# Kernel tuning notes

Measured on AMD Instinct MI355X. Metric: run time of the kernel, lower is better.

The kernel has to match this reference:

```python
import jax, jax.numpy as jnp
import numpy as np

B = 16384
F_CONT = 128   # continuous features (Gaussian scopes)
F_CAT = 128    # integer-valued features (Categorical scopes)
NG = 1024      # number of Gaussian leaves
NC = 1024      # number of Categorical leaves
K = 32         # categorical classes
LOG_2PI = float(np.log(2.0 * np.pi))


def setup_inputs() -> dict:
    key = jax.random.key(0)
    k1, k2, k3, k4, k5, k6, k7 = jax.random.split(key, 7)
    # data: first F_CONT columns continuous, last F_CAT columns hold integer category values
    x_cont = jax.random.normal(k1, (B, F_CONT), dtype=jnp.float32)
    x_cat = jax.random.randint(k2, (B, F_CAT), 0, K).astype(jnp.float32)
    x = jnp.concatenate([x_cont, x_cat], axis=1)  # [B, 256]
    gauss_mean = jax.random.normal(k3, (NG,), dtype=jnp.float32)
    gauss_std = jax.random.uniform(k4, (NG,), dtype=jnp.float32, minval=0.5, maxval=2.0)
    cat_logp = jax.nn.log_softmax(jax.random.normal(k5, (NC, K), dtype=jnp.float32), axis=-1)
    gauss_scopes = jax.random.randint(k6, (NG,), 0, F_CONT)            # index into continuous cols
    cat_scopes = jax.random.randint(k7, (NC,), 0, F_CAT) + F_CONT      # index into categorical cols
    return {
        "x": x,
        "gauss_mean": gauss_mean,
        "gauss_std": gauss_std,
        "cat_logp": cat_logp,
        "gauss_scopes": gauss_scopes,
        "cat_scopes": cat_scopes,
    }


def reference(x, gauss_mean, gauss_std, cat_logp, gauss_scopes, cat_scopes):
    # Fused equivalent of the per-leaf Python loop: one gather + one formula per family.
    # Gaussian leaves: Normal(mean, std).log_prob(x[:, scope])
    gv = x[:, gauss_scopes]                                   # [B, NG]
    z = (gv - gauss_mean[None, :]) / gauss_std[None, :]
    g_ll = -0.5 * (z * z) - jnp.log(gauss_std)[None, :] - 0.5 * LOG_2PI
    # Categorical leaves: log p_i[x[:, scope_i]]
    cidx = x[:, cat_scopes].astype(jnp.int32)                 # [B, NC]
    c_ll = cat_logp[jnp.arange(cat_logp.shape[0])[None, :], cidx]  # [B, NC]
    return jnp.concatenate([g_ll, c_ll], axis=1)              # [B, NG+NC]
```

## Files before the change

### kernel.cpp

```cpp
#include <hip/hip_runtime.h>
#include <math.h>


#define HALF_LOG_2PI 0.91893853320467274178f

constexpr int BROWS   = 16384;
constexpr int FX      = 256;
constexpr int NG      = 1024;
constexpr int NC      = 1024;
constexpr int KCAT    = 32;
constexpr int OUTW    = NG + NC;
constexpr int ROWS_PB = 16;
constexpr int NTHR    = 256;
constexpr int XPITCH  = FX + 1;
constexpr int CCH     = 128;
constexpr int NCHUNK  = NC / CCH;
constexpr int TPITCH  = 36;

__global__ __launch_bounds__(NTHR) void leaves_kernel(
    const float* __restrict__ x,
    const float* __restrict__ gmean,
    const float* __restrict__ gstd,
    const float* __restrict__ clogp,
    const int*   __restrict__ gsc,
    const int*   __restrict__ csc,
    float*       __restrict__ out)
{
    __shared__ float xs[ROWS_PB * XPITCH];
    __shared__ float wt[4][ROWS_PB * TPITCH];

    const int t = threadIdx.x;
    const long long b0 = (long long)blockIdx.x * ROWS_PB;

    {
        const int r  = t >> 4;
        const int c0 = (t & 15) * 16;
        const float* src = x + (b0 + r) * FX + c0;
        float*       dst = xs + r * XPITCH + c0;
        #pragma unroll
        for (int q = 0; q < 4; ++q) {
            float4 v = ((const float4*)src)[q];
            dst[q * 4 + 0] = v.x; dst[q * 4 + 1] = v.y;
            dst[q * 4 + 2] = v.z; dst[q * 4 + 3] = v.w;
        }
    }

    const int4   g4 = ((const int4*)gsc)[t];
    const float4 mu = ((const float4*)gmean)[t];
    const float4 sd = ((const float4*)gstd)[t];
    float4 is, cc;
    is.x = 1.0f / sd.x;  cc.x = -logf(sd.x) - HALF_LOG_2PI;
    is.y = 1.0f / sd.y;  cc.y = -logf(sd.y) - HALF_LOG_2PI;
    is.z = 1.0f / sd.z;  cc.z = -logf(sd.z) - HALF_LOG_2PI;
    is.w = 1.0f / sd.w;  cc.w = -logf(sd.w) - HALF_LOG_2PI;

    __syncthreads();

    #pragma unroll
    for (int r = 0; r < ROWS_PB; ++r) {
        const float* xr = xs + r * XPITCH;
        float4 gres;
        { float z = (xr[g4.x] - mu.x) * is.x; gres.x = fmaf(-0.5f * z, z, cc.x); }
        { float z = (xr[g4.y] - mu.y) * is.y; gres.y = fmaf(-0.5f * z, z, cc.y); }
        { float z = (xr[g4.z] - mu.z) * is.z; gres.z = fmaf(-0.5f * z, z, cc.z); }
        { float z = (xr[g4.w] - mu.w) * is.w; gres.w = fmaf(-0.5f * z, z, cc.w); }
        ((float4*)(out + (b0 + r) * OUTW))[t] = gres;
    }

    const int w    = t >> 6;
    const int l    = t & 63;
    const int grow = l & 15;
    const int gco  = l >> 4;
    const int frow = l >> 2;
    const int fol  = l & 3;
    float*       tile = wt[w];
    const float* xrp  = xs + grow * XPITCH;

    for (int chunk = 0; chunk < NCHUNK; ++chunk) {
        const int cb = chunk * CCH + w * 32 + gco;

        float v[8];
        #pragma unroll
        for (int j = 0; j < 8; ++j) {
            const int c = cb + j * 4;
            v[j] = clogp[c * KCAT + (int)xrp[csc[c]]];
        }

        #pragma unroll
        for (int j = 0; j < 8; ++j)
            tile[grow * TPITCH + j * 4 + gco] = v[j];

        const float* trow = tile + frow * TPITCH;
        float*       drow = out + (b0 + frow) * OUTW + NG + chunk * CCH + w * 32;
        #pragma unroll
        for (int q = 0; q < 2; ++q) {
            float4 a = *(const float4*)(trow + q * 16 + fol * 4);
            *(float4*)(drow + q * 16 + fol * 4) = a;
        }
    }
}

extern "C" void kernel_launch(void* const* d_in, const int* in_sizes, int n_in,
                              void* d_out, int out_size, void* d_ws, size_t ws_size,
                              hipStream_t stream) {
    const float* x     = (const float*)d_in[0];
    const float* gmean = (const float*)d_in[1];
    const float* gstd  = (const float*)d_in[2];
    const float* clogp = (const float*)d_in[3];
    const int*   gsc   = (const int*)d_in[4];
    const int*   csc   = (const int*)d_in[5];
    float*       out   = (float*)d_out;

    leaves_kernel<<<dim3(BROWS / ROWS_PB), dim3(NTHR), 0, stream>>>(
        x, gmean, gstd, clogp, gsc, csc, out);
}
```

Before: 30.81 us.

## Stage categorical outputs in a block-wide shared tile and write full 512-column rows

Replaces the per-wave 32-column transpose tiles with one shared tile covering 512 categorical columns for all 16 rows, filled in two passes. Each pass issues 32 independent gathers per thread before storing, which raises memory-level parallelism. Stores then go out as contiguous 2KB row segments rather than 128-byte pieces. In exchange it uses more registers and more shared memory (about 36KB more) and adds block-wide barriers, which may lower occupancy.

```diff
diff --git a/kernel.cpp b/kernel.cpp
--- a/kernel.cpp
+++ b/kernel.cpp
@@ -3,6 +3,8 @@
 
 
 #define HALF_LOG_2PI 0.91893853320467274178f
+
+typedef float f32x4 __attribute__((ext_vector_type(4)));
 
 constexpr int BROWS   = 16384;
 constexpr int FX      = 256;
@@ -13,9 +15,8 @@
 constexpr int ROWS_PB = 16;
 constexpr int NTHR    = 256;
 constexpr int XPITCH  = FX + 1;
-constexpr int CCH     = 128;
-constexpr int NCHUNK  = NC / CCH;
-constexpr int TPITCH  = 36;
+constexpr int HCOLS   = 512;
+constexpr int TP      = 572;
 
 __global__ __launch_bounds__(NTHR) void leaves_kernel(
     const float* __restrict__ x,
@@ -27,7 +28,7 @@
     float*       __restrict__ out)
 {
     __shared__ float xs[ROWS_PB * XPITCH];
-    __shared__ float wt[4][ROWS_PB * TPITCH];
+    __shared__ float tile[ROWS_PB * TP];
 
     const int t = threadIdx.x;
     const long long b0 = (long long)blockIdx.x * ROWS_PB;
@@ -48,11 +49,11 @@
     const int4   g4 = ((const int4*)gsc)[t];
     const float4 mu = ((const float4*)gmean)[t];
     const float4 sd = ((const float4*)gstd)[t];
-    float4 is, cc;
-    is.x = 1.0f / sd.x;  cc.x = -logf(sd.x) - HALF_LOG_2PI;
-    is.y = 1.0f / sd.y;  cc.y = -logf(sd.y) - HALF_LOG_2PI;
-    is.z = 1.0f / sd.z;  cc.z = -logf(sd.z) - HALF_LOG_2PI;
-    is.w = 1.0f / sd.w;  cc.w = -logf(sd.w) - HALF_LOG_2PI;
+    float4 is, cc4;
+    is.x = 1.0f / sd.x;  cc4.x = -logf(sd.x) - HALF_LOG_2PI;
+    is.y = 1.0f / sd.y;  cc4.y = -logf(sd.y) - HALF_LOG_2PI;
+    is.z = 1.0f / sd.z;  cc4.z = -logf(sd.z) - HALF_LOG_2PI;
+    is.w = 1.0f / sd.w;  cc4.w = -logf(sd.w) - HALF_LOG_2PI;
 
     __syncthreads();
 
@@ -60,10 +61,10 @@
     for (int r = 0; r < ROWS_PB; ++r) {
         const float* xr = xs + r * XPITCH;
         float4 gres;
-        { float z = (xr[g4.x] - mu.x) * is.x; gres.x = fmaf(-0.5f * z, z, cc.x); }
-        { float z = (xr[g4.y] - mu.y) * is.y; gres.y = fmaf(-0.5f * z, z, cc.y); }
-        { float z = (xr[g4.z] - mu.z) * is.z; gres.z = fmaf(-0.5f * z, z, cc.z); }
-        { float z = (xr[g4.w] - mu.w) * is.w; gres.w = fmaf(-0.5f * z, z, cc.w); }
+        { float z = (xr[g4.x] - mu.x) * is.x; gres.x = fmaf(-0.5f * z, z, cc4.x); }
+        { float z = (xr[g4.y] - mu.y) * is.y; gres.y = fmaf(-0.5f * z, z, cc4.y); }
+        { float z = (xr[g4.z] - mu.z) * is.z; gres.z = fmaf(-0.5f * z, z, cc4.z); }
+        { float z = (xr[g4.w] - mu.w) * is.w; gres.w = fmaf(-0.5f * z, z, cc4.w); }
         ((float4*)(out + (b0 + r) * OUTW))[t] = gres;
     }
 
@@ -71,31 +72,44 @@
     const int l    = t & 63;
     const int grow = l & 15;
     const int gco  = l >> 4;
-    const int frow = l >> 2;
-    const int fol  = l & 3;
-    float*       tile = wt[w];
-    const float* xrp  = xs + grow * XPITCH;
+    const float* xrp = xs + grow * XPITCH;
 
-    for (int chunk = 0; chunk < NCHUNK; ++chunk) {
-        const int cb = chunk * CCH + w * 32 + gco;
+    const int frsub = t >> 7;
+    const int fcol  = (t & 127) * 4;
+    const int fcadr = ((fcol >> 5) * 36) + (fcol & 31);
 
-        float v[8];
+    #pragma unroll
+    for (int pass = 0; pass < 2; ++pass) {
+        const int cpb = pass * HCOLS + w * 32 + gco;
+
+        float v[32];
         #pragma unroll
-        for (int j = 0; j < 8; ++j) {
-            const int c = cb + j * 4;
-            v[j] = clogp[c * KCAT + (int)xrp[csc[c]]];
+        for (int cc = 0; cc < 4; ++cc) {
+            #pragma unroll
+            for (int jj = 0; jj < 8; ++jj) {
+                const int c = cpb + cc * 128 + jj * 4;
+                v[cc * 8 + jj] = clogp[c * KCAT + (int)xrp[csc[c]]];
+            }
         }
 
+        __syncthreads();
+
         #pragma unroll
-        for (int j = 0; j < 8; ++j)
-            tile[grow * TPITCH + j * 4 + gco] = v[j];
+        for (int cc = 0; cc < 4; ++cc) {
+            #pragma unroll
+            for (int jj = 0; jj < 8; ++jj) {
+                const int C = cc * 128 + w * 32 + jj * 4 + gco;
+                tile[grow * TP + ((C >> 5) * 36) + (C & 31)] = v[cc * 8 + jj];
+            }
+        }
 
-        const float* trow = tile + frow * TPITCH;
-        float*       drow = out + (b0 + frow) * OUTW + NG + chunk * CCH + w * 32;
+        __syncthreads();
+
         #pragma unroll
-        for (int q = 0; q < 2; ++q) {
-            float4 a = *(const float4*)(trow + q * 16 + fol * 4);
-            *(float4*)(drow + q * 16 + fol * 4) = a;
+        for (int s = 0; s < 8; ++s) {
+            const int r = s * 2 + frsub;
+            f32x4 a = *(const f32x4*)(tile + r * TP + fcadr);
+            *(f32x4*)(out + (b0 + r) * OUTW + NG + pass * HCOLS + fcol) = a;
         }
     }
 }
```

Measured after the change: 32.66 us. 6.0% more time.
